# Kernel tuning notes

Measured on AMD Instinct MI355X. Metric: run time of the kernel, lower is better.

The kernel has to match this reference:

```python
import jax, jax.numpy as jnp
import numpy as np

HEADS = 8

def setup_inputs() -> dict:
    key = jax.random.key(0)
    ks = jax.random.split(key, 5)
    B, C, H, W = 2, 256, 64, 64
    dim = C
    x = jax.random.normal(ks[0], (B, C, H, W), dtype=jnp.float32)
    # Linear weights stored as [in, out] so y = x @ W + b
    w_qkv = jax.random.normal(ks[1], (dim, 3 * dim), dtype=jnp.float32) * (dim ** -0.5)
    b_qkv = jax.random.normal(ks[2], (3 * dim,), dtype=jnp.float32) * 0.02
    w_out = jax.random.normal(ks[3], (dim, dim), dtype=jnp.float32) * (dim ** -0.5)
    b_out = jax.random.normal(ks[4], (dim,), dtype=jnp.float32) * 0.02
    return {"x": x, "w_qkv": w_qkv, "b_qkv": b_qkv, "w_out": w_out, "b_out": b_out}

def reference(x, w_qkv, b_qkv, w_out, b_out):
    B, C, H, W = x.shape
    h = HEADS
    d = C // h
    scale = d ** -0.5
    # [B, C, H, W] -> [B, N, C]
    tokens = x.reshape(B, C, H * W).transpose(0, 2, 1)
    qkv = tokens @ w_qkv + b_qkv  # [B, N, 3C]
    q, k, v = jnp.split(qkv, 3, axis=-1)
    def to_heads(t):
        Bn, N, _ = t.shape
        return t.reshape(Bn, N, h, d).transpose(0, 2, 1, 3)  # [B, h, N, d]
    q, k, v = map(to_heads, (q, k, v))
    dots = jnp.einsum('bhnd,bhmd->bhnm', q, k) * scale  # [B, h, N, N]
    attn = jax.nn.softmax(dots, axis=-1)
    out = jnp.einsum('bhnm,bhmd->bhnd', attn, v)  # [B, h, N, d]
    out = out.transpose(0, 2, 1, 3).reshape(B, H * W, C)  # [B, N, C]
    out = out @ w_out + b_out
    return out.transpose(0, 2, 1).reshape(B, C, H, W)
```

## Files before the change

kernel.cpp:

```cpp
#include <hip/hip_runtime.h>

typedef __attribute__((ext_vector_type(8))) short s16x8;
typedef __attribute__((ext_vector_type(4))) float f32x4;
typedef __attribute__((ext_vector_type(16))) float f32x16;
typedef __attribute__((ext_vector_type(2))) unsigned u32x2;
typedef __attribute__((ext_vector_type(4))) unsigned u32x4;

#define MFMA32(a, b, c) __builtin_amdgcn_mfma_f32_16x16x32_bf16((a), (b), (c), 0, 0, 0)

#if __has_builtin(__builtin_amdgcn_mfma_f32_32x32x16_bf16)
#define MFMA3216(a, b, c) __builtin_amdgcn_mfma_f32_32x32x16_bf16((a), (b), (c), 0, 0, 0)
#else
#define MFMA3216(a, b, c) (c)
#endif

#if __has_builtin(__builtin_amdgcn_exp2f)
#define EXP2F(x) __builtin_amdgcn_exp2f(x)
#else
#define EXP2F(x) __exp2f(x)
#endif

#if __has_builtin(__builtin_amdgcn_rcpf)
#define RCPF(x) __builtin_amdgcn_rcpf(x)
#else
#define RCPF(x) (1.0f / (x))
#endif

#define SL2E 0.25507313f

__device__ __forceinline__ unsigned pkrne(float a, float b) {
  unsigned ua = __builtin_bit_cast(unsigned, a);
  unsigned ub = __builtin_bit_cast(unsigned, b);
  ua += 0x7FFFu + ((ua >> 16) & 1u);
  ub += 0x7FFFu + ((ub >> 16) & 1u);
  return __builtin_amdgcn_perm(ub, ua, 0x07060302u);
}

__device__ __forceinline__ unsigned pktrunc(float a, float b) {
  return __builtin_amdgcn_perm(__builtin_bit_cast(unsigned, b),
                               __builtin_bit_cast(unsigned, a), 0x07060302u);
}

__device__ __forceinline__ unsigned short bfr(float f) {
  unsigned u = __builtin_bit_cast(unsigned, f);
  u += 0x7FFFu + ((u >> 16) & 1u);
  return (unsigned short)(u >> 16);
}

__device__ __forceinline__ float bflo(unsigned u) {
  return __builtin_bit_cast(float, u << 16);
}
__device__ __forceinline__ float bfhi(unsigned u) {
  return __builtin_bit_cast(float, u & 0xFFFF0000u);
}

__device__ __forceinline__ u32x2 plswap(unsigned a, unsigned b) {
#if __has_builtin(__builtin_amdgcn_permlane32_swap)
  return __builtin_amdgcn_permlane32_swap(a, b, false, false);
#else
  unsigned sa = (unsigned)__shfl_xor((int)a, 32, 64);
  unsigned sb = (unsigned)__shfl_xor((int)b, 32, 64);
  bool hi = (threadIdx.x & 63) >= 32;
  u32x2 r;
  r.x = hi ? sb : a;
  r.y = hi ? b : sa;
  return r;
#endif
}

__device__ __forceinline__ void stage16(const ushort* g, ushort* l, int lane) {
#if __has_builtin(__builtin_amdgcn_global_load_lds)
  __builtin_amdgcn_global_load_lds(
      (__attribute__((address_space(1))) unsigned int*)(unsigned long long)(
          const void*)g,
      (__attribute__((address_space(3))) unsigned int*)(unsigned)(
          unsigned long long)(const void*)l,
      16, 0, 0);
#else
  *(uint4*)(l + lane * 8) = *(const uint4*)g;
#endif
}

__global__ __launch_bounds__(256) void prep_kernel(
    const float* __restrict__ x, const float* __restrict__ wqkv,
    const float* __restrict__ wout, ushort* __restrict__ xbf,
    ushort* __restrict__ wT, ushort* __restrict__ woT) {
  const int t = threadIdx.x;
  const int sub = t & 15, grp = t >> 4;
  const int id = blockIdx.x;
  const float* src;
  ushort* dst;
  int src_ld, k0, n0;
  float sc = 1.f;
  if (id < 512) {
    int mt = id & 63, kt = (id >> 6) & 3, b = id >> 8;
    src = x + (size_t)b * 256 * 4096;
    src_ld = 4096;
    dst = xbf + (size_t)b * 4096 * 256;
    k0 = kt * 64;
    n0 = mt * 64;
  } else if (id < 560) {
    int r = id - 512, nt = r % 12, kt = r / 12;
    src = wqkv;
    src_ld = 768;
    dst = wT;
    k0 = kt * 64;
    n0 = nt * 64;
    if (n0 < 256) sc = SL2E;
  } else {
    int r = id - 560, nt = r & 3, kt = r >> 2;
    src = wout;
    src_ld = 256;
    dst = woT;
    k0 = kt * 64;
    n0 = nt * 64;
  }
  const int k = k0 + grp * 4;
  const int n = n0 + sub * 4;
  unsigned d0[4], d1[4];
#pragma unroll
  for (int i = 0; i < 4; ++i) {
    float4 v = *(const float4*)(src + (size_t)(k + i) * src_ld + n);
    d0[i] = pkrne(v.x * sc, v.y * sc);
    d1[i] = pkrne(v.z * sc, v.w * sc);
  }
  u32x2 r0 = {__builtin_amdgcn_perm(d0[1], d0[0], 0x05040100u),
              __builtin_amdgcn_perm(d0[3], d0[2], 0x05040100u)};
  u32x2 r1 = {__builtin_amdgcn_perm(d0[1], d0[0], 0x07060302u),
              __builtin_amdgcn_perm(d0[3], d0[2], 0x07060302u)};
  u32x2 r2 = {__builtin_amdgcn_perm(d1[1], d1[0], 0x05040100u),
              __builtin_amdgcn_perm(d1[3], d1[2], 0x05040100u)};
  u32x2 r3 = {__builtin_amdgcn_perm(d1[1], d1[0], 0x07060302u),
              __builtin_amdgcn_perm(d1[3], d1[2], 0x07060302u)};
  *(u32x2*)(dst + (size_t)(n + 0) * 256 + k) = r0;
  *(u32x2*)(dst + (size_t)(n + 1) * 256 + k) = r1;
  *(u32x2*)(dst + (size_t)(n + 2) * 256 + k) = r2;
  *(u32x2*)(dst + (size_t)(n + 3) * 256 + k) = r3;
}

__global__ __launch_bounds__(256) void qkv_kernel(
    const ushort* __restrict__ xbf, const ushort* __restrict__ wT,
    const float* __restrict__ bq, ushort* __restrict__ QG,
    ushort* __restrict__ KG, ushort* __restrict__ VtG) {
  __shared__ __align__(16) ushort Wl[64][40];
  __shared__ __align__(16) ushort Xl[128][40];
  const int t0 = blockIdx.x * 128;
  const int n0 = blockIdx.y * 64;
  const int t = threadIdx.x;
  const int wid = t >> 6, lane = t & 63;
  const int wy = wid >> 1, wx = wid & 1;
  const int quad = lane >> 4, l16 = lane & 15;
  f32x4 acc[2][4] = {};
  const int wr = t >> 2, wsg = t & 3;
  for (int k0 = 0; k0 < 256; k0 += 32) {
    __syncthreads();
    *(uint4*)&Wl[wr][wsg * 8] =
        *(const uint4*)(wT + (size_t)(n0 + wr) * 256 + k0 + wsg * 8);
#pragma unroll
    for (int i = 0; i < 2; ++i) {
      int fid = t + 256 * i, row = fid >> 2, seg = fid & 3;
      *(uint4*)&Xl[row][seg * 8] =
          *(const uint4*)(xbf + (size_t)(t0 + row) * 256 + k0 + seg * 8);
    }
    __syncthreads();
    s16x8 wf[2], xf[4];
#pragma unroll
    for (int i = 0; i < 2; ++i)
      wf[i] = *(const s16x8*)&Wl[32 * wy + 16 * i + l16][quad * 8];
#pragma unroll
    for (int j = 0; j < 4; ++j)
      xf[j] = *(const s16x8*)&Xl[64 * wx + 16 * j + l16][quad * 8];
#pragma unroll
    for (int i = 0; i < 2; ++i)
#pragma unroll
      for (int j = 0; j < 4; ++j) acc[i][j] = MFMA32(wf[i], xf[j], acc[i][j]);
  }
  if (n0 < 512) {
    ushort* dst = (n0 < 256) ? QG : KG;
    const float bsc = (n0 < 256) ? SL2E : 1.f;
#pragma unroll
    for (int i = 0; i < 2; ++i) {
      int nb = n0 + 32 * wy + 16 * i + 4 * quad;
      float4 b4 = *(const float4*)(bq + nb);
      float bx0 = b4.x * bsc, bx1 = b4.y * bsc, bx2 = b4.z * bsc,
            bx3 = b4.w * bsc;
      int h = ((nb & 255) >> 5);
      int dd0 = nb & 31;
#pragma unroll
      for (int j = 0; j < 4; ++j) {
        int tok = t0 + 64 * wx + 16 * j + l16;
        int b = tok >> 12, tokn = tok & 4095;
        u32x2 pk = {pkrne(acc[i][j][0] + bx0, acc[i][j][1] + bx1),
                    pkrne(acc[i][j][2] + bx2, acc[i][j][3] + bx3)};
        *(u32x2*)(dst + ((size_t)(b * 8 + h) * 4096 + tokn) * 32 + dd0) = pk;
      }
    }
  } else {
#pragma unroll
    for (int i = 0; i < 2; ++i) {
      int nb = n0 + 32 * wy + 16 * i + 4 * quad;
      float4 b4 = *(const float4*)(bq + nb);
      float bb[4] = {b4.x, b4.y, b4.z, b4.w};
#pragma unroll
      for (int r = 0; r < 4; ++r) {
        int nn = nb + r - 512;
        int h = nn >> 5, ddv = nn & 31;
        ushort* vrow = VtG + (size_t)(h * 32 + ddv) * 4096;
#pragma unroll
        for (int j = 0; j < 4; ++j) {
          int tok = t0 + 64 * wx + 16 * j + l16;
          int b = tok >> 12, tokn = tok & 4095;
          vrow[(size_t)b * 8 * 32 * 4096 + tokn] = bfr(acc[i][j][r] + bb[r]);
        }
      }
    }
  }
}

__global__ __launch_bounds__(256, 4) void attn_split(
    const ushort* __restrict__ QG, const ushort* __restrict__ KG,
    const ushort* __restrict__ VtG, ushort* __restrict__ OF0,
    ushort* __restrict__ OFb, float* __restrict__ LF) {
  __shared__ __align__(64) ushort KVs[2][4096];
  const int id = blockIdx.x;
  const int bh = (id & 7) * 2 + ((id >> 3) & 1);
  const int q0 = ((id >> 4) & 31) * 128;
  const int sp = id >> 9;
  const int kt0 = sp * 32;
  const int niter = 32;
  const int t = threadIdx.x;
  const int wid = t >> 6, lane = t & 63;
  const int l5 = lane & 31, hi = lane >> 5;
  const size_t base = (size_t)bh * 4096 * 32;
  const ushort* qp = QG + base;
  const ushort* kp = KG + base;
  const ushort* vp = VtG + base;
  const int qw = q0 + 32 * wid;
  const ushort* qrow = qp + (size_t)(qw + l5) * 32 + hi * 8;
  const s16x8 qf0 = *(const s16x8*)(qrow);
  const s16x8 qf1 = *(const s16x8*)(qrow + 16);
  const int sK = wid >> 1, hK = wid & 1;
  const int kdst = sK * 1024 + hK * 512;
  const ushort* kpre =
      kp + (size_t)(kt0 * 64 + sK * 32 + l5) * 32 + hK * 16 + hi * 8;
  const ushort* vpre =
      vp + (size_t)l5 * 4096 + kt0 * 64 + sK * 32 + hK * 16 + hi * 8;
  stage16(kpre, &KVs[0][kdst], lane);
  stage16(vpre, &KVs[0][2048 + kdst], lane);
  kpre += 2048;
  vpre += 64;
  __syncthreads();
  f32x16 o = {};
  f32x16 o_l = {};
  const s16x8 ones8 = {(short)0x3F80, (short)0x3F80, (short)0x3F80,
                       (short)0x3F80, (short)0x3F80, (short)0x3F80,
                       (short)0x3F80, (short)0x3F80};
  for (int i = 0; i < niter; ++i) {
    const int cur = i & 1;
    if (i + 1 < niter) {
      stage16(kpre, &KVs[cur ^ 1][kdst], lane);
      stage16(vpre, &KVs[cur ^ 1][2048 + kdst], lane);
      kpre += 2048;
      vpre += 64;
    }
    const ushort* kb = &KVs[cur][0];
    const ushort* vb = &KVs[cur][2048];
#pragma unroll
    for (int s = 0; s < 2; ++s) {
      const s16x8 ka0 = *(const s16x8*)(kb + s * 1024 + lane * 8);
      const s16x8 ka1 = *(const s16x8*)(kb + s * 1024 + 512 + lane * 8);
      f32x16 S = {};
      S = MFMA3216(ka0, qf0, S);
      S = MFMA3216(ka1, qf1, S);
      unsigned w8[8];
#pragma unroll
      for (int ii = 0; ii < 8; ++ii)
        w8[ii] = pktrunc(EXP2F(S[2 * ii]), EXP2F(S[2 * ii + 1]));
      u32x2 sw0 = plswap(w8[0], w8[2]);
      u32x2 sw1 = plswap(w8[1], w8[3]);
      u32x2 sw2 = plswap(w8[4], w8[6]);
      u32x2 sw3 = plswap(w8[5], w8[7]);
      u32x4 pa0 = {sw0.x, sw1.x, sw0.y, sw1.y};
      u32x4 pa1 = {sw2.x, sw3.x, sw2.y, sw3.y};
      const s16x8 pA0 = __builtin_bit_cast(s16x8, pa0);
      const s16x8 pA1 = __builtin_bit_cast(s16x8, pa1);
      const s16x8 va0 = *(const s16x8*)(vb + s * 1024 + lane * 8);
      const s16x8 va1 = *(const s16x8*)(vb + s * 1024 + 512 + lane * 8);
      o = MFMA3216(pA0, va0, o);
      o = MFMA3216(pA1, va1, o);
      o_l = MFMA3216(pA0, ones8, o_l);
      o_l = MFMA3216(pA1, ones8, o_l);
    }
    __syncthreads();
  }
  ushort* OFs = (sp == 0) ? OF0 : OFb;
  float* LFs = LF + (size_t)sp * 65536;
#pragma unroll
  for (int r = 0; r < 16; ++r) {
    int q = qw + (r & 3) + 8 * (r >> 2) + 4 * hi;
    OFs[((size_t)bh * 4096 + q) * 32 + l5] = bfr(o[r]);
  }
  float lval = o_l[0];
#pragma unroll
  for (int r = 1; r < 16; ++r) lval = (l5 == r) ? o_l[r] : lval;
  if (l5 < 16)
    LFs[(size_t)bh * 4096 + qw + (l5 & 3) + 8 * (l5 >> 2) + 4 * hi] = lval;
}

__global__ __launch_bounds__(256) void proj_split(
    const ushort* __restrict__ OF0, const ushort* __restrict__ OFb,
    const float* __restrict__ LF, const ushort* __restrict__ woT,
    const float* __restrict__ bo, float* __restrict__ out) {
  __shared__ __align__(16) ushort Wl[64][40];
  __shared__ __align__(16) ushort Xl[128][40];
  const int t0 = blockIdx.x * 128;
  const int c0 = blockIdx.y * 64;
  const int t = threadIdx.x;
  const int wid = t >> 6, lane = t & 63;
  const int wy = wid >> 1, wx = wid & 1;
  const int quad = lane >> 4, l16 = lane & 15;
  f32x4 acc[2][4] = {};
  const int wr = t >> 2, wsg = t & 3;
  const int c8 = (t & 7) * 4;
  for (int k0 = 0; k0 < 256; k0 += 32) {
    __syncthreads();
    *(uint4*)&Wl[wr][wsg * 8] =
        *(const uint4*)(woT + (size_t)(c0 + wr) * 256 + k0 + wsg * 8);
    const int hh = k0 >> 5;
#pragma unroll
    for (int p = 0; p < 4; ++p) {
      int row = 32 * p + (t >> 3);
      int tok = t0 + row, bb = tok >> 12, tokn = tok & 4095;
      size_t ro = (size_t)(bb * 8 + hh) * 4096 + tokn;
      size_t oi = ro * 32 + c8;
      uint2 a0 = *(const uint2*)(OF0 + oi);
      uint2 a1 = *(const uint2*)(OFb + oi);
      float l = LF[ro] + LF[65536 + ro];
      float inv = RCPF(l);
      f32x4 s;
      s[0] = bflo(a0.x) + bflo(a1.x);
      s[1] = bfhi(a0.x) + bfhi(a1.x);
      s[2] = bflo(a0.y) + bflo(a1.y);
      s[3] = bfhi(a0.y) + bfhi(a1.y);
      s *= inv;
      u32x2 pk = {pkrne(s[0], s[1]), pkrne(s[2], s[3])};
      *(u32x2*)&Xl[row][c8] = pk;
    }
    __syncthreads();
    s16x8 wf[2], xf[4];
#pragma unroll
    for (int i = 0; i < 2; ++i)
      wf[i] = *(const s16x8*)&Wl[32 * wy + 16 * i + l16][quad * 8];
#pragma unroll
    for (int j = 0; j < 4; ++j)
      xf[j] = *(const s16x8*)&Xl[64 * wx + 16 * j + l16][quad * 8];
#pragma unroll
    for (int i = 0; i < 2; ++i)
#pragma unroll
      for (int j = 0; j < 4; ++j) acc[i][j] = MFMA32(wf[i], xf[j], acc[i][j]);
  }
#pragma unroll
  for (int i = 0; i < 2; ++i) {
    int cb = c0 + 32 * wy + 16 * i + 4 * quad;
    float4 b4 = *(const float4*)(bo + cb);
    float bb[4] = {b4.x, b4.y, b4.z, b4.w};
#pragma unroll
    for (int j = 0; j < 4; ++j) {
      int tok = t0 + 64 * wx + 16 * j + l16;
      int b = tok >> 12, tokn = tok & 4095;
#pragma unroll
      for (int r = 0; r < 4; ++r)
        out[((size_t)(b * 256 + cb + r)) * 4096 + tokn] = acc[i][j][r] + bb[r];
    }
  }
}

extern "C" void kernel_launch(void* const* d_in, const int* in_sizes, int n_in,
                              void* d_out, int out_size, void* d_ws, size_t ws_size,
                              hipStream_t stream) {
  (void)in_sizes; (void)n_in; (void)out_size; (void)ws_size;
  const float* x = (const float*)d_in[0];
  const float* wq = (const float*)d_in[1];
  const float* bq = (const float*)d_in[2];
  const float* wo = (const float*)d_in[3];
  const float* bo = (const float*)d_in[4];
  float* out = (float*)d_out;
  ushort* ws = (ushort*)d_ws;
  ushort* xbf = ws;
  ushort* OF0 = ws;
  ushort* QG  = ws + 2097152;
  ushort* KG  = ws + 4194304;
  ushort* VtG = ws + 6291456;
  ushort* wT  = ws + 8388608;
  ushort* woT = ws + 8585216;
  ushort* OFb = ws + 8650752;
  float* LF = (float*)(ws + 12845056);
  prep_kernel<<<576, 256, 0, stream>>>(x, wq, wo, xbf, wT, woT);
  qkv_kernel<<<dim3(64, 12), 256, 0, stream>>>(xbf, wT, bq, QG, KG, VtG);
  attn_split<<<1024, 256, 0, stream>>>(QG, KG, VtG, OF0, OFb, LF);
  proj_split<<<dim3(64, 4), 256, 0, stream>>>(OF0, OFb, LF, woT, bo, out);
}
```

Baseline: 139.7 us.

## Store K and V in MFMA fragment order and load directly from global

The QKV projection now writes K and V tiles already arranged in the per-lane MFMA fragment layout. This lets the attention kernel read its K/V operands straight from global memory with contiguous 16-byte loads per lane. The LDS double-buffering and the per-iteration __syncthreads are removed. In exchange, each of the four waves in a block reads the same K/V tile separately from global/L2 instead of sharing one LDS copy, and there is no explicit prefetch to hide load latency. The V transpose store also becomes a scattered 2-byte write pattern.

```diff
diff --git a/kernel.cpp b/kernel.cpp
--- a/kernel.cpp
+++ b/kernel.cpp
@@ -65,19 +65,6 @@
   r.x = hi ? sb : a;
   r.y = hi ? b : sa;
   return r;
-#endif
-}
-
-__device__ __forceinline__ void stage16(const ushort* g, ushort* l, int lane) {
-#if __has_builtin(__builtin_amdgcn_global_load_lds)
-  __builtin_amdgcn_global_load_lds(
-      (__attribute__((address_space(1))) unsigned int*)(unsigned long long)(
-          const void*)g,
-      (__attribute__((address_space(3))) unsigned int*)(unsigned)(
-          unsigned long long)(const void*)l,
-      16, 0, 0);
-#else
-  *(uint4*)(l + lane * 8) = *(const uint4*)g;
 #endif
 }
 
@@ -175,15 +162,13 @@
 #pragma unroll
       for (int j = 0; j < 4; ++j) acc[i][j] = MFMA32(wf[i], xf[j], acc[i][j]);
   }
-  if (n0 < 512) {
-    ushort* dst = (n0 < 256) ? QG : KG;
-    const float bsc = (n0 < 256) ? SL2E : 1.f;
+  if (n0 < 256) {
 #pragma unroll
     for (int i = 0; i < 2; ++i) {
       int nb = n0 + 32 * wy + 16 * i + 4 * quad;
       float4 b4 = *(const float4*)(bq + nb);
-      float bx0 = b4.x * bsc, bx1 = b4.y * bsc, bx2 = b4.z * bsc,
-            bx3 = b4.w * bsc;
+      float bx0 = b4.x * SL2E, bx1 = b4.y * SL2E, bx2 = b4.z * SL2E,
+            bx3 = b4.w * SL2E;
       int h = ((nb & 255) >> 5);
       int dd0 = nb & 31;
 #pragma unroll
@@ -192,7 +177,26 @@
         int b = tok >> 12, tokn = tok & 4095;
         u32x2 pk = {pkrne(acc[i][j][0] + bx0, acc[i][j][1] + bx1),
                     pkrne(acc[i][j][2] + bx2, acc[i][j][3] + bx3)};
-        *(u32x2*)(dst + ((size_t)(b * 8 + h) * 4096 + tokn) * 32 + dd0) = pk;
+        *(u32x2*)(QG + ((size_t)(b * 8 + h) * 4096 + tokn) * 32 + dd0) = pk;
+      }
+    }
+  } else if (n0 < 512) {
+#pragma unroll
+    for (int i = 0; i < 2; ++i) {
+      int nb = n0 + 32 * wy + 16 * i + 4 * quad;
+      float4 b4 = *(const float4*)(bq + nb);
+      float bx0 = b4.x, bx1 = b4.y, bx2 = b4.z, bx3 = b4.w;
+      int h = ((nb & 255) >> 5);
+      size_t fo = (size_t)i * 512 + (quad >> 1) * 256 + (quad & 1) * 4;
+#pragma unroll
+      for (int j = 0; j < 4; ++j) {
+        int tok = t0 + 64 * wx + 16 * j + l16;
+        int b = tok >> 12, tokn = tok & 4095;
+        int tl = tokn >> 6, ss = (tokn >> 5) & 1, l5 = tokn & 31;
+        u32x2 pk = {pkrne(acc[i][j][0] + bx0, acc[i][j][1] + bx1),
+                    pkrne(acc[i][j][2] + bx2, acc[i][j][3] + bx3)};
+        *(u32x2*)(KG + (size_t)(b * 8 + h) * 131072 + (size_t)tl * 2048 +
+                  ss * 1024 + l5 * 8 + fo) = pk;
       }
     }
   } else {
@@ -204,13 +208,15 @@
 #pragma unroll
       for (int r = 0; r < 4; ++r) {
         int nn = nb + r - 512;
-        int h = nn >> 5, ddv = nn & 31;
-        ushort* vrow = VtG + (size_t)(h * 32 + ddv) * 4096;
+        int h = nn >> 5, d = nn & 31;
 #pragma unroll
         for (int j = 0; j < 4; ++j) {
           int tok = t0 + 64 * wx + 16 * j + l16;
           int b = tok >> 12, tokn = tok & 4095;
-          vrow[(size_t)b * 8 * 32 * 4096 + tokn] = bfr(acc[i][j][r] + bb[r]);
+          int tl = tokn >> 6, ss = (tokn >> 5) & 1;
+          int hV = (tokn >> 4) & 1, hii = (tokn >> 3) & 1, e = tokn & 7;
+          VtG[(size_t)(b * 8 + h) * 131072 + (size_t)tl * 2048 + ss * 1024 +
+              hV * 512 + hii * 256 + d * 8 + e] = bfr(acc[i][j][r] + bb[r]);
         }
       }
     }
@@ -221,7 +227,6 @@
     const ushort* __restrict__ QG, const ushort* __restrict__ KG,
     const ushort* __restrict__ VtG, ushort* __restrict__ OF0,
     ushort* __restrict__ OFb, float* __restrict__ LF) {
-  __shared__ __align__(64) ushort KVs[2][4096];
   const int id = blockIdx.x;
   const int bh = (id & 7) * 2 + ((id >> 3) & 1);
   const int q0 = ((id >> 4) & 31) * 128;
@@ -231,44 +236,36 @@
   const int t = threadIdx.x;
   const int wid = t >> 6, lane = t & 63;
   const int l5 = lane & 31, hi = lane >> 5;
-  const size_t base = (size_t)bh * 4096 * 32;
-  const ushort* qp = QG + base;
-  const ushort* kp = KG + base;
-  const ushort* vp = VtG + base;
+  const ushort* qp = QG + (size_t)bh * 4096 * 32;
+  const ushort* kgp = KG + (size_t)bh * 131072 + (size_t)kt0 * 2048;
+  const ushort* vgp = VtG + (size_t)bh * 131072 + (size_t)kt0 * 2048;
   const int qw = q0 + 32 * wid;
   const ushort* qrow = qp + (size_t)(qw + l5) * 32 + hi * 8;
   const s16x8 qf0 = *(const s16x8*)(qrow);
   const s16x8 qf1 = *(const s16x8*)(qrow + 16);
-  const int sK = wid >> 1, hK = wid & 1;
-  const int kdst = sK * 1024 + hK * 512;
-  const ushort* kpre =
-      kp + (size_t)(kt0 * 64 + sK * 32 + l5) * 32 + hK * 16 + hi * 8;
-  const ushort* vpre =
-      vp + (size_t)l5 * 4096 + kt0 * 64 + sK * 32 + hK * 16 + hi * 8;
-  stage16(kpre, &KVs[0][kdst], lane);
-  stage16(vpre, &KVs[0][2048 + kdst], lane);
-  kpre += 2048;
-  vpre += 64;
-  __syncthreads();
   f32x16 o = {};
   f32x16 o_l = {};
   const s16x8 ones8 = {(short)0x3F80, (short)0x3F80, (short)0x3F80,
                        (short)0x3F80, (short)0x3F80, (short)0x3F80,
                        (short)0x3F80, (short)0x3F80};
+  const int lo8 = lane * 8;
   for (int i = 0; i < niter; ++i) {
-    const int cur = i & 1;
-    if (i + 1 < niter) {
-      stage16(kpre, &KVs[cur ^ 1][kdst], lane);
-      stage16(vpre, &KVs[cur ^ 1][2048 + kdst], lane);
-      kpre += 2048;
-      vpre += 64;
-    }
-    const ushort* kb = &KVs[cur][0];
-    const ushort* vb = &KVs[cur][2048];
+    const ushort* kt = kgp + (size_t)i * 2048;
+    const ushort* vt = vgp + (size_t)i * 2048;
+    s16x8 k00 = *(const s16x8*)(kt + lo8);
+    s16x8 k01 = *(const s16x8*)(kt + 512 + lo8);
+    s16x8 v00 = *(const s16x8*)(vt + lo8);
+    s16x8 v01 = *(const s16x8*)(vt + 512 + lo8);
+    s16x8 k10 = *(const s16x8*)(kt + 1024 + lo8);
+    s16x8 k11 = *(const s16x8*)(kt + 1536 + lo8);
+    s16x8 v10 = *(const s16x8*)(vt + 1024 + lo8);
+    s16x8 v11 = *(const s16x8*)(vt + 1536 + lo8);
 #pragma unroll
     for (int s = 0; s < 2; ++s) {
-      const s16x8 ka0 = *(const s16x8*)(kb + s * 1024 + lane * 8);
-      const s16x8 ka1 = *(const s16x8*)(kb + s * 1024 + 512 + lane * 8);
+      const s16x8 ka0 = s ? k10 : k00;
+      const s16x8 ka1 = s ? k11 : k01;
+      const s16x8 va0 = s ? v10 : v00;
+      const s16x8 va1 = s ? v11 : v01;
       f32x16 S = {};
       S = MFMA3216(ka0, qf0, S);
       S = MFMA3216(ka1, qf1, S);
@@ -284,14 +281,11 @@
       u32x4 pa1 = {sw2.x, sw3.x, sw2.y, sw3.y};
       const s16x8 pA0 = __builtin_bit_cast(s16x8, pa0);
       const s16x8 pA1 = __builtin_bit_cast(s16x8, pa1);
-      const s16x8 va0 = *(const s16x8*)(vb + s * 1024 + lane * 8);
-      const s16x8 va1 = *(const s16x8*)(vb + s * 1024 + 512 + lane * 8);
       o = MFMA3216(pA0, va0, o);
       o = MFMA3216(pA1, va1, o);
       o_l = MFMA3216(pA0, ones8, o_l);
       o_l = MFMA3216(pA1, ones8, o_l);
     }
-    __syncthreads();
   }
   ushort* OFs = (sp == 0) ? OF0 : OFb;
   float* LFs = LF + (size_t)sp * 65536;
```

Measured after the change: 143.4 us. +2.7%, slower.
